# Optimization experiments

Hardware: AMD Instinct MI355X
Metric: run time of the kernel (lower is better)

Reference implementation:

```python
import jax, jax.numpy as jnp
import numpy as np

K = 20  # number of nearest neighbors (includes self, distance 0, as in torch topk(largest=False))


def edge_feature(x, k):
    """x: (B, C, N) -> edge features (B, N, k, 2C) = concat[central, neighbor - central]."""
    sq = jnp.sum(x * x, axis=1)                       # (B, N)
    inner = jnp.einsum('bcn,bcm->bnm', x, x)          # (B, N, N)
    d = sq[:, :, None] + sq[:, None, :] - 2.0 * inner # squared pairwise distance
    _, idx = jax.lax.top_k(-d, k)                     # (B, N, k) nearest indices (incl. self)
    xT = jnp.transpose(x, (0, 2, 1))                  # (B, N, C)
    # nb[b,n,j,c] = xT[b, idx[b,n,j], c]
    nb = jnp.take_along_axis(xT[:, :, None, :], idx[:, :, :, None], axis=1)  # (B, N, k, C)
    central = jnp.broadcast_to(xT[:, :, None, :], nb.shape)
    return jnp.concatenate([central, nb - central], axis=-1)  # (B, N, k, 2C)


def setup_inputs() -> dict:
    key = jax.random.key(0)
    ks = jax.random.split(key, 13)
    B, C, N = 8, 3, 4096
    def w(k_, shape, fan_in):
        return (jax.random.normal(k_, shape, dtype=jnp.float32) / np.sqrt(fan_in)).astype(jnp.float32)
    inp = {
        'x':  jax.random.normal(ks[0], (B, C, N), dtype=jnp.float32),
        # local 1x1 conv2d weights (out_ch, in_ch)
        'W1': w(ks[1], (64, 6), 6),        'b1': jnp.zeros((64,), jnp.float32),
        'W2': w(ks[2], (128, 64), 64),     'b2': jnp.zeros((128,), jnp.float32),
        # inter 1x1 conv1d
        'W3': w(ks[3], (1024, 128), 128),  'b3': jnp.zeros((1024,), jnp.float32),
        # global FC
        'W4': w(ks[4], (512, 1024), 1024), 'b4': jnp.zeros((512,), jnp.float32),
        'W5': w(ks[5], (256, 512), 512),   'b5': jnp.zeros((256,), jnp.float32),
        # final linear (torch inits this to zeros -> identity output; use small random for a
        # non-trivial correctness baseline, same math path)
        'W6': 0.01 * w(ks[6], (9, 256), 256), 'b6': jnp.zeros((9,), jnp.float32),
    }
    return inp


def reference(x, W1, b1, W2, b2, W3, b3, W4, b4, W5, b5, W6, b6):
    e = edge_feature(x, K)                                     # (B, N, k, 6)
    h = jax.nn.relu(jnp.einsum('bnkc,oc->bnko', e, W1) + b1)   # (B, N, k, 64)
    h = jax.nn.relu(jnp.einsum('bnkc,oc->bnko', h, W2) + b2)   # (B, N, k, 128)
    h = jnp.max(h, axis=2)                                     # max over k -> (B, N, 128)
    h = jax.nn.relu(jnp.einsum('bnc,oc->bno', h, W3) + b3)     # (B, N, 1024)
    g = jnp.max(h, axis=1)                                     # max over points -> (B, 1024)
    g = jax.nn.relu(g @ W4.T + b4)                             # (B, 512)
    g = jax.nn.relu(g @ W5.T + b5)                             # (B, 256)
    t = g @ W6.T + b6                                          # (B, 9)
    Bsz = x.shape[0]
    out_ch, in_ch = 3, 3
    t = t.reshape(Bsz, out_ch, in_ch) + jnp.eye(out_ch, in_ch, dtype=t.dtype)
    return t
```

## Files before the change

### kernel.cpp

```cpp
#include <hip/hip_runtime.h>
#include <hip/hip_bf16.h>
#include <cstdint>

#define B_SZ 8
#define NPTS 4096
#define KNN  20
#define NTOT (B_SZ * NPTS)
#define PPB  8

typedef unsigned int uint;
typedef unsigned short ushort;
using short8 = __attribute__((ext_vector_type(8))) short;
using f32x4  = __attribute__((ext_vector_type(4))) float;

__device__ __forceinline__ ushort f2bf(float f) {
  uint u = __float_as_uint(f);
  u += 0x7fff + ((u >> 16) & 1);
  return (ushort)(u >> 16);
}
__device__ __forceinline__ float bf2f(ushort h) {
  return __uint_as_float(((uint)h) << 16);
}

__global__ __launch_bounds__(256) void prep_kernel(const float* __restrict__ x,
                                                   const float* __restrict__ W1,
                                                   const float* __restrict__ W3,
                                                   const float* __restrict__ W2,
                                                   ushort* __restrict__ u,
                                                   ushort* __restrict__ W3b,
                                                   ushort* __restrict__ W2b) {
  int blk = blockIdx.x;
  if (blk < 1024) {
    int t = blk * 256 + threadIdx.x;
    int p = t >> 3, c0 = (t & 7) * 8;
    int b = p >> 12, n = p & (NPTS - 1);
    const float* xb = x + (size_t)b * 3 * NPTS;
    float x0 = xb[n], x1 = xb[NPTS + n], x2 = xb[2 * NPTS + n];
    uint pk[4];
    #pragma unroll
    for (int j = 0; j < 8; ++j) {
      const float* w = W1 + (c0 + j) * 6;
      float v = w[3] * x0 + w[4] * x1 + w[5] * x2;
      ushort h = f2bf(v);
      if (j & 1) pk[j >> 1] |= ((uint)h << 16); else pk[j >> 1] = h;
    }
    uint4 q; q.x = pk[0]; q.y = pk[1]; q.z = pk[2]; q.w = pk[3];
    *reinterpret_cast<uint4*>(u + (size_t)p * 64 + c0) = q;
  } else if (blk < 1088) {
    int t = (blk - 1024) * 256 + threadIdx.x;
    const float4* src = reinterpret_cast<const float4*>(W3 + t * 8);
    float4 f0 = src[0], f1 = src[1];
    uint4 pk;
    pk.x = (uint)f2bf(f0.x) | ((uint)f2bf(f0.y) << 16);
    pk.y = (uint)f2bf(f0.z) | ((uint)f2bf(f0.w) << 16);
    pk.z = (uint)f2bf(f1.x) | ((uint)f2bf(f1.y) << 16);
    pk.w = (uint)f2bf(f1.z) | ((uint)f2bf(f1.w) << 16);
    *reinterpret_cast<uint4*>(W3b + t * 8) = pk;
  } else {
    int t = (blk - 1088) * 256 + threadIdx.x;
    const float4* src = reinterpret_cast<const float4*>(W2 + t * 8);
    float4 f0 = src[0], f1 = src[1];
    uint4 pk;
    pk.x = (uint)f2bf(f0.x) | ((uint)f2bf(f0.y) << 16);
    pk.y = (uint)f2bf(f0.z) | ((uint)f2bf(f0.w) << 16);
    pk.z = (uint)f2bf(f1.x) | ((uint)f2bf(f1.y) << 16);
    pk.w = (uint)f2bf(f1.z) | ((uint)f2bf(f1.w) << 16);
    *reinterpret_cast<uint4*>(W2b + t * 8) = pk;
  }
}

__device__ __forceinline__ void sortf64(float& v, int lane) {
  #pragma unroll
  for (int k = 2; k <= 64; k <<= 1) {
    #pragma unroll
    for (int j = k >> 1; j > 0; j >>= 1) {
      float o = __shfl_xor(v, j, 64);
      bool keepmin = (((lane & k) == 0) == ((lane & j) == 0));
      bool lt = v < o;
      v = (keepmin == lt) ? v : o;
    }
  }
}

__device__ __forceinline__ void sortu64(unsigned long long& v, int lane) {
  #pragma unroll
  for (int k = 2; k <= 64; k <<= 1) {
    #pragma unroll
    for (int j = k >> 1; j > 0; j >>= 1) {
      unsigned long long o = __shfl_xor(v, j, 64);
      bool keepmin = (((lane & k) == 0) == ((lane & j) == 0));
      bool lt = v < o;
      v = (keepmin == lt) ? v : o;
    }
  }
}

__global__ __launch_bounds__(256, 4) void knn_kernel(const float* __restrict__ x,
                                                     int* __restrict__ idx_out) {
  __shared__ int surv[4][256];
  __shared__ int cnt[4];
  const unsigned long long INFK = ~0ull;
  int w = threadIdx.x >> 6, lane = threadIdx.x & 63;
  int row = blockIdx.x * 4 + w;
  int b = row >> 12, n = row & (NPTS - 1);
  const float* xb = x + (size_t)b * 3 * NPTS;
  float qx = xb[n], qy = xb[NPTS + n], qz = xb[2 * NPTS + n];
  if (lane == 0) cnt[w] = 0;

  const float4* X0 = reinterpret_cast<const float4*>(xb);
  const float4* X1 = reinterpret_cast<const float4*>(xb + NPTS);
  const float4* X2 = reinterpret_cast<const float4*>(xb + 2 * NPTS);

  uint kreg[32];
  float bm = 3.0e38f;
  #pragma unroll
  for (int i = 0; i < 16; ++i) {
    int v4 = i * 64 + lane;
    float4 a0 = X0[v4], a1 = X1[v4], a2 = X2[v4];
    float dx, dy, dz, d0, d1, d2, d3;
    dx = a0.x - qx; dy = a1.x - qy; dz = a2.x - qz; d0 = dx*dx + dy*dy + dz*dz;
    dx = a0.y - qx; dy = a1.y - qy; dz = a2.y - qz; d1 = dx*dx + dy*dy + dz*dz;
    dx = a0.z - qx; dy = a1.z - qy; dz = a2.z - qz; d2 = dx*dx + dy*dy + dz*dz;
    dx = a0.w - qx; dy = a1.w - qy; dz = a2.w - qz; d3 = dx*dx + dy*dy + dz*dz;
    bm = fminf(bm, fminf(fminf(d0, d1), fminf(d2, d3)));
    kreg[2*i]   = (__float_as_uint(d0) >> 16) | (__float_as_uint(d1) & 0xFFFF0000u);
    kreg[2*i+1] = (__float_as_uint(d2) >> 16) | (__float_as_uint(d3) & 0xFFFF0000u);
  }

  sortf64(bm, lane);
  float T = __shfl(bm, 19, 64);
  uint T16 = __float_as_uint(T) >> 16;

  asm volatile("s_waitcnt lgkmcnt(0)" ::: "memory");
  #pragma unroll
  for (int i = 0; i < 16; ++i) {
    uint ka = kreg[2*i], kb = kreg[2*i+1];
    int m0 = (i * 64 + lane) * 4;
    if ((ka & 0xffffu) <= T16) { int s = atomicAdd(&cnt[w], 1); if (s < 256) surv[w][s] = m0; }
    if ((ka >> 16)     <= T16) { int s = atomicAdd(&cnt[w], 1); if (s < 256) surv[w][s] = m0 + 1; }
    if ((kb & 0xffffu) <= T16) { int s = atomicAdd(&cnt[w], 1); if (s < 256) surv[w][s] = m0 + 2; }
    if ((kb >> 16)     <= T16) { int s = atomicAdd(&cnt[w], 1); if (s < 256) surv[w][s] = m0 + 3; }
  }
  asm volatile("s_waitcnt lgkmcnt(0)" ::: "memory");
  int M = cnt[w];

  if (M <= 256) {
    unsigned long long run = INFK;
    int nch = (M + 63) >> 6;
    for (int c = 0; c < nch; ++c) {
      int s = c * 64 + lane;
      unsigned long long v = INFK;
      if (s < M) {
        int m = surv[w][s];
        float dx = xb[m] - qx, dy = xb[NPTS + m] - qy, dz = xb[2 * NPTS + m] - qz;
        float d = dx * dx + dy * dy + dz * dz;
        v = ((unsigned long long)__float_as_uint(d) << 32) | (unsigned)m;
      }
      sortu64(v, lane);
      if (c == 0) {
        run = v;
      } else {
        unsigned long long b19 = __shfl(v, (19 - lane) & 63, 64);
        unsigned long long cand = run < b19 ? run : b19;
        run = (lane < KNN) ? cand : INFK;
        sortu64(run, lane);
      }
    }
    if (lane < KNN) idx_out[(size_t)row * KNN + lane] = (int)(run & 0xFFFFFFFFull);
  } else {
    unsigned long long prev = 0ull;
    for (int r = 0; r < KNN; ++r) {
      unsigned long long best = INFK;
      for (int i = 0; i < 16; ++i) {
        int v4 = i * 64 + lane;
        float4 a0 = X0[v4], a1 = X1[v4], a2 = X2[v4];
        float dx, dy, dz, d[4];
        dx = a0.x - qx; dy = a1.x - qy; dz = a2.x - qz; d[0] = dx*dx + dy*dy + dz*dz;
        dx = a0.y - qx; dy = a1.y - qy; dz = a2.y - qz; d[1] = dx*dx + dy*dy + dz*dz;
        dx = a0.z - qx; dy = a1.z - qy; dz = a2.z - qz; d[2] = dx*dx + dy*dy + dz*dz;
        dx = a0.w - qx; dy = a1.w - qy; dz = a2.w - qz; d[3] = dx*dx + dy*dy + dz*dz;
        #pragma unroll
        for (int j = 0; j < 4; ++j) {
          int m = i * 256 + lane * 4 + j;
          unsigned long long key =
              ((unsigned long long)__float_as_uint(d[j]) << 32) | (unsigned)m;
          if ((r == 0 || key > prev) && key < best) best = key;
        }
      }
      #pragma unroll
      for (int off = 32; off; off >>= 1) {
        unsigned long long o = __shfl_xor(best, off, 64);
        best = o < best ? o : best;
      }
      if (lane == 0) idx_out[(size_t)row * KNN + r] = (int)(best & 0xFFFFFFFFull);
      prev = best;
    }
  }
}

__global__ __launch_bounds__(256, 4) void edge_kernel(
    const float* __restrict__ x,  const float* __restrict__ W1, const float* __restrict__ b1,
    const ushort* __restrict__ W2b, const float* __restrict__ b2,
    const ushort* __restrict__ u, const int* __restrict__ idx,
    float* __restrict__ h128) {
  __shared__ __align__(16) char h1s[PPB * 32 * 128];
  __shared__ float vs[PPB * 64];
  __shared__ int   nbs[PPB * KNN];

  int tid = threadIdx.x, w = tid >> 6, l = tid & 63;
  int p0 = blockIdx.x * PPB;
  int b = p0 >> 12;
  const float* xb = x + (size_t)b * 3 * NPTS;

  for (int t = tid; t < PPB * 64; t += 256) {
    int p = t >> 6, c = t & 63;
    int n = (p0 + p) & (NPTS - 1);
    float x0 = xb[n], x1 = xb[NPTS + n], x2 = xb[2 * NPTS + n];
    const float* wr = W1 + c * 6;
    vs[t] = (wr[0] - wr[3]) * x0 + (wr[1] - wr[4]) * x1 + (wr[2] - wr[5]) * x2 + b1[c];
  }
  if (tid < PPB * KNN) nbs[tid] = idx[(size_t)p0 * KNN + tid];

  short8 bfr[8][2];
  #pragma unroll
  for (int nt = 0; nt < 8; ++nt) {
    #pragma unroll
    for (int ks = 0; ks < 2; ++ks) {
      bfr[nt][ks] = *(const short8*)(W2b + (nt * 16 + (l & 15)) * 64
                                         + ks * 32 + (l >> 4) * 8);
    }
  }
  __syncthreads();

  const ushort* ub = u + (((size_t)b) << 12) * 64;
  #pragma unroll
  for (int j = 0; j < 8; ++j) {
    int e_loc = j * 8 + (l >> 3);
    int p_loc = (w << 1) + (e_loc >> 5);
    int e_in = e_loc & 31;
    int e_src = (e_in < KNN) ? e_in : e_in - KNN;
    int nb = nbs[p_loc * KNN + e_src];
    int c0 = (l & 7) * 8;
    uint4 uv = *(const uint4*)(ub + (((size_t)nb) << 6) + c0);
    const float* vp = vs + p_loc * 64 + c0;
    float4 v0 = *(const float4*)vp, v1 = *(const float4*)(vp + 4);
    float h0 = fmaxf(bf2f((ushort)(uv.x & 0xffff)) + v0.x, 0.f);
    float h1 = fmaxf(bf2f((ushort)(uv.x >> 16))    + v0.y, 0.f);
    float h2 = fmaxf(bf2f((ushort)(uv.y & 0xffff)) + v0.z, 0.f);
    float h3 = fmaxf(bf2f((ushort)(uv.y >> 16))    + v0.w, 0.f);
    float h4 = fmaxf(bf2f((ushort)(uv.z & 0xffff)) + v1.x, 0.f);
    float h5 = fmaxf(bf2f((ushort)(uv.z >> 16))    + v1.y, 0.f);
    float h6 = fmaxf(bf2f((ushort)(uv.w & 0xffff)) + v1.z, 0.f);
    float h7 = fmaxf(bf2f((ushort)(uv.w >> 16))    + v1.w, 0.f);
    uint4 pk;
    pk.x = (uint)f2bf(h0) | ((uint)f2bf(h1) << 16);
    pk.y = (uint)f2bf(h2) | ((uint)f2bf(h3) << 16);
    pk.z = (uint)f2bf(h4) | ((uint)f2bf(h5) << 16);
    pk.w = (uint)f2bf(h6) | ((uint)f2bf(h7) << 16);
    int row = (w << 6) + e_loc;
    int byte = (row * 128 + c0 * 2) ^ ((row & 7) << 4);
    *(uint4*)(h1s + byte) = pk;
  }
  __syncthreads();

  float bias0 = b2[l], bias1 = b2[64 + l];

  #pragma unroll
  for (int pt = 0; pt < 2; ++pt) {
    int rbase = (w << 6) + (pt << 5);
    short8 a[2][2];
    #pragma unroll
    for (int m = 0; m < 2; ++m) {
      #pragma unroll
      for (int ks = 0; ks < 2; ++ks) {
        int row = rbase + m * 16 + (l & 15);
        int byte = (row * 128 + ks * 64 + (l >> 4) * 16) ^ ((row & 7) << 4);
        a[m][ks] = *(const short8*)(h1s + byte);
      }
    }
    float r03 = 0.f, r47 = 0.f;
    #pragma unroll
    for (int nt = 0; nt < 8; ++nt) {
      f32x4 acc0 = {0.f, 0.f, 0.f, 0.f}, acc1 = {0.f, 0.f, 0.f, 0.f};
      acc0 = __builtin_amdgcn_mfma_f32_16x16x32_bf16(a[0][0], bfr[nt][0], acc0, 0, 0, 0);
      acc0 = __builtin_amdgcn_mfma_f32_16x16x32_bf16(a[0][1], bfr[nt][1], acc0, 0, 0, 0);
      acc1 = __builtin_amdgcn_mfma_f32_16x16x32_bf16(a[1][0], bfr[nt][0], acc1, 0, 0, 0);
      acc1 = __builtin_amdgcn_mfma_f32_16x16x32_bf16(a[1][1], bfr[nt][1], acc1, 0, 0, 0);
      float m0 = fmaxf(fmaxf(fmaxf(acc0[0], acc1[0]), fmaxf(acc0[1], acc1[1])),
                       fmaxf(fmaxf(acc0[2], acc1[2]), fmaxf(acc0[3], acc1[3])));
      m0 = fmaxf(m0, __shfl_xor(m0, 16, 64));
      m0 = fmaxf(m0, __shfl_xor(m0, 32, 64));
      if ((l >> 4) == (nt & 3)) { if (nt < 4) r03 = m0; else r47 = m0; }
    }
    int pg = p0 + (w << 1) + pt;
    h128[(size_t)pg * 128 + l]      = fmaxf(r03 + bias0, 0.f);
    h128[(size_t)pg * 128 + 64 + l] = fmaxf(r47 + bias1, 0.f);
  }
}

__global__ __launch_bounds__(256, 2) void inter_kernel(
    const float* __restrict__ h128, const ushort* __restrict__ W3b,
    float* __restrict__ partial) {
  __shared__ __align__(16) char as_[32 * 256];
  int tid = threadIdx.x, w = tid >> 6, l = tid & 63;
  int chunk = blockIdx.x;
  const float* hp = h128 + (size_t)chunk * 32 * 128;

  {
    int row = tid >> 3, c0 = (tid & 7) * 16;
    const float4* src = reinterpret_cast<const float4*>(hp + row * 128 + c0);
    float4 f0 = src[0], f1 = src[1], f2 = src[2], f3 = src[3];
    uint4 p0, p1;
    p0.x = (uint)f2bf(f0.x) | ((uint)f2bf(f0.y) << 16);
    p0.y = (uint)f2bf(f0.z) | ((uint)f2bf(f0.w) << 16);
    p0.z = (uint)f2bf(f1.x) | ((uint)f2bf(f1.y) << 16);
    p0.w = (uint)f2bf(f1.z) | ((uint)f2bf(f1.w) << 16);
    p1.x = (uint)f2bf(f2.x) | ((uint)f2bf(f2.y) << 16);
    p1.y = (uint)f2bf(f2.z) | ((uint)f2bf(f2.w) << 16);
    p1.z = (uint)f2bf(f3.x) | ((uint)f2bf(f3.y) << 16);
    p1.w = (uint)f2bf(f3.z) | ((uint)f2bf(f3.w) << 16);
    int sw = (row & 7) << 4;
    *(uint4*)(as_ + ((row * 256 + c0 * 2) ^ sw))      = p0;
    *(uint4*)(as_ + ((row * 256 + c0 * 2 + 16) ^ sw)) = p1;
  }
  __syncthreads();

  short8 a[2][4];
  #pragma unroll
  for (int m = 0; m < 2; ++m) {
    #pragma unroll
    for (int ks = 0; ks < 4; ++ks) {
      int row = m * 16 + (l & 15);
      int byte = (row * 256 + ks * 64 + (l >> 4) * 16) ^ ((row & 7) << 4);
      a[m][ks] = *(const short8*)(as_ + byte);
    }
  }

  const ushort* wb = W3b + (size_t)(w * 256) * 128;
  float res[4];
  #pragma unroll
  for (int nt = 0; nt < 16; ++nt) {
    f32x4 acc0 = {0.f, 0.f, 0.f, 0.f}, acc1 = {0.f, 0.f, 0.f, 0.f};
    #pragma unroll
    for (int ks = 0; ks < 4; ++ks) {
      short8 bf = *(const short8*)(wb + (size_t)(nt * 16 + (l & 15)) * 128
                                      + ks * 32 + (l >> 4) * 8);
      acc0 = __builtin_amdgcn_mfma_f32_16x16x32_bf16(a[0][ks], bf, acc0, 0, 0, 0);
      acc1 = __builtin_amdgcn_mfma_f32_16x16x32_bf16(a[1][ks], bf, acc1, 0, 0, 0);
    }
    float m0 = fmaxf(fmaxf(fmaxf(acc0[0], acc1[0]), fmaxf(acc0[1], acc1[1])),
                     fmaxf(fmaxf(acc0[2], acc1[2]), fmaxf(acc0[3], acc1[3])));
    m0 = fmaxf(m0, __shfl_xor(m0, 16, 64));
    m0 = fmaxf(m0, __shfl_xor(m0, 32, 64));
    if ((l >> 4) == (nt & 3)) res[nt >> 2] = m0;
  }
  float* pp = partial + (size_t)chunk * 1024 + w * 256;
  #pragma unroll
  for (int g = 0; g < 4; ++g) pp[g * 64 + l] = res[g];
}

__global__ __launch_bounds__(256) void gmax_kernel(const float* __restrict__ partial,
                                                   const float* __restrict__ b3,
                                                   float* __restrict__ g) {
  int t = blockIdx.x * 256 + threadIdx.x;
  if (t >= B_SZ * 1024) return;
  int b = t >> 10, ch = t & 1023;
  const float* p = partial + (size_t)b * 128 * 1024 + ch;
  float m = -3.0e38f;
  for (int i = 0; i < 128; ++i) m = fmaxf(m, p[(size_t)i * 1024]);
  g[t] = fmaxf(m + b3[ch], 0.0f);
}

__global__ __launch_bounds__(64) void fc_kernel(const float* __restrict__ in,
                                                const float* __restrict__ W,
                                                const float* __restrict__ bias,
                                                float* __restrict__ out,
                                                int in_dim, int out_dim, int mode) {
  int blk = blockIdx.x;
  int b = blk / out_dim, o = blk % out_dim;
  int lane = threadIdx.x;
  const float* iv = in + (size_t)b * in_dim;
  const float* w  = W  + (size_t)o * in_dim;
  float s = 0.f;
  for (int c = lane; c < in_dim; c += 64) s += iv[c] * w[c];
  #pragma unroll
  for (int off = 32; off; off >>= 1) s += __shfl_down(s, off);
  if (lane == 0) {
    float r = s + bias[o];
    if (mode == 0) r = fmaxf(r, 0.0f);
    else if (o == 0 || o == 4 || o == 8) r += 1.0f;
    out[blk] = r;
  }
}

extern "C" void kernel_launch(void* const* d_in, const int* in_sizes, int n_in,
                              void* d_out, int out_size, void* d_ws, size_t ws_size,
                              hipStream_t stream) {
  const float* x  = (const float*)d_in[0];
  const float* W1 = (const float*)d_in[1];
  const float* b1 = (const float*)d_in[2];
  const float* W2 = (const float*)d_in[3];
  const float* b2 = (const float*)d_in[4];
  const float* W3 = (const float*)d_in[5];
  const float* b3 = (const float*)d_in[6];
  const float* W4 = (const float*)d_in[7];
  const float* b4 = (const float*)d_in[8];
  const float* W5 = (const float*)d_in[9];
  const float* b5 = (const float*)d_in[10];
  const float* W6 = (const float*)d_in[11];
  const float* b6 = (const float*)d_in[12];
  float* out = (float*)d_out;

  char* ws = (char*)d_ws;
  ushort* u_bf = (ushort*)(ws);
  int*   idxb  = (int*)  (ws + (8u  << 20));
  float* h128  = (float*)(ws + (11u << 20));
  ushort* W3b  = (ushort*)(ws + (27u << 20));
  ushort* W2b  = (ushort*)(ws + (27u << 20) + (256u << 10));
  float* part  = (float*)(ws);
  float* g     = (float*)(ws + (5u  << 20));
  float* g4    = (float*)(ws + (6u  << 20));
  float* g5    = (float*)(ws + (7u  << 20));

  hipLaunchKernelGGL(prep_kernel, dim3(1092), dim3(256), 0, stream,
                     x, W1, W3, W2, u_bf, W3b, W2b);
  hipLaunchKernelGGL(knn_kernel,  dim3(8192), dim3(256), 0, stream, x, idxb);
  hipLaunchKernelGGL(edge_kernel, dim3(NTOT / PPB), dim3(256), 0, stream,
                     x, W1, b1, W2b, b2, u_bf, idxb, h128);
  hipLaunchKernelGGL(inter_kernel, dim3(1024), dim3(256), 0, stream, h128, W3b, part);
  hipLaunchKernelGGL(gmax_kernel, dim3(32), dim3(256), 0, stream, part, b3, g);
  hipLaunchKernelGGL(fc_kernel, dim3(B_SZ * 512), dim3(64), 0, stream, g,  W4, b4, g4, 1024, 512, 0);
  hipLaunchKernelGGL(fc_kernel, dim3(B_SZ * 256), dim3(64), 0, stream, g4, W5, b5, g5, 512, 256, 0);
  hipLaunchKernelGGL(fc_kernel, dim3(B_SZ * 9),   dim3(64), 0, stream, g5, W6, b6, out, 256, 9, 1);
}
```

Before: 187.9 us.

## Fuse prep into knn launch and replace gmax kernel with atomicMax reduction

Folds the bf16 prep work into extra blocks of the knn kernel launch, so one launch is removed. The inter kernel now reduces its per-chunk maxima straight into a global buffer with atomicMax on order-preserving encoded floats, which removes the partial buffer and the separate gmax kernel. The bias and ReLU from gmax move into the first FC kernel, which decodes the values as it loads them. This adds a memset launch and atomic contention on 8K addresses, 128 chunks per batch.

```diff
diff --git a/kernel.cpp b/kernel.cpp
--- a/kernel.cpp
+++ b/kernel.cpp
@@ -21,52 +21,13 @@
 __device__ __forceinline__ float bf2f(ushort h) {
   return __uint_as_float(((uint)h) << 16);
 }
-
-__global__ __launch_bounds__(256) void prep_kernel(const float* __restrict__ x,
-                                                   const float* __restrict__ W1,
-                                                   const float* __restrict__ W3,
-                                                   const float* __restrict__ W2,
-                                                   ushort* __restrict__ u,
-                                                   ushort* __restrict__ W3b,
-                                                   ushort* __restrict__ W2b) {
-  int blk = blockIdx.x;
-  if (blk < 1024) {
-    int t = blk * 256 + threadIdx.x;
-    int p = t >> 3, c0 = (t & 7) * 8;
-    int b = p >> 12, n = p & (NPTS - 1);
-    const float* xb = x + (size_t)b * 3 * NPTS;
-    float x0 = xb[n], x1 = xb[NPTS + n], x2 = xb[2 * NPTS + n];
-    uint pk[4];
-    #pragma unroll
-    for (int j = 0; j < 8; ++j) {
-      const float* w = W1 + (c0 + j) * 6;
-      float v = w[3] * x0 + w[4] * x1 + w[5] * x2;
-      ushort h = f2bf(v);
-      if (j & 1) pk[j >> 1] |= ((uint)h << 16); else pk[j >> 1] = h;
-    }
-    uint4 q; q.x = pk[0]; q.y = pk[1]; q.z = pk[2]; q.w = pk[3];
-    *reinterpret_cast<uint4*>(u + (size_t)p * 64 + c0) = q;
-  } else if (blk < 1088) {
-    int t = (blk - 1024) * 256 + threadIdx.x;
-    const float4* src = reinterpret_cast<const float4*>(W3 + t * 8);
-    float4 f0 = src[0], f1 = src[1];
-    uint4 pk;
-    pk.x = (uint)f2bf(f0.x) | ((uint)f2bf(f0.y) << 16);
-    pk.y = (uint)f2bf(f0.z) | ((uint)f2bf(f0.w) << 16);
-    pk.z = (uint)f2bf(f1.x) | ((uint)f2bf(f1.y) << 16);
-    pk.w = (uint)f2bf(f1.z) | ((uint)f2bf(f1.w) << 16);
-    *reinterpret_cast<uint4*>(W3b + t * 8) = pk;
-  } else {
-    int t = (blk - 1088) * 256 + threadIdx.x;
-    const float4* src = reinterpret_cast<const float4*>(W2 + t * 8);
-    float4 f0 = src[0], f1 = src[1];
-    uint4 pk;
-    pk.x = (uint)f2bf(f0.x) | ((uint)f2bf(f0.y) << 16);
-    pk.y = (uint)f2bf(f0.z) | ((uint)f2bf(f0.w) << 16);
-    pk.z = (uint)f2bf(f1.x) | ((uint)f2bf(f1.y) << 16);
-    pk.w = (uint)f2bf(f1.z) | ((uint)f2bf(f1.w) << 16);
-    *reinterpret_cast<uint4*>(W2b + t * 8) = pk;
-  }
+__device__ __forceinline__ uint fenc(float f) {
+  uint u = __float_as_uint(f);
+  return (u & 0x80000000u) ? ~u : (u | 0x80000000u);
+}
+__device__ __forceinline__ float fdec(uint e) {
+  uint u = (e & 0x80000000u) ? (e & 0x7fffffffu) : ~e;
+  return __uint_as_float(u);
 }
 
 __device__ __forceinline__ void sortf64(float& v, int lane) {
@@ -95,10 +56,56 @@
   }
 }
 
-__global__ __launch_bounds__(256, 4) void knn_kernel(const float* __restrict__ x,
-                                                     int* __restrict__ idx_out) {
+__global__ __launch_bounds__(256, 4) void knn_prep_kernel(
+    const float* __restrict__ x,  const float* __restrict__ W1,
+    const float* __restrict__ W3, const float* __restrict__ W2,
+    ushort* __restrict__ u, ushort* __restrict__ W3b, ushort* __restrict__ W2b,
+    int* __restrict__ idx_out) {
   __shared__ int surv[4][256];
   __shared__ int cnt[4];
+
+  if (blockIdx.x >= 8192) {
+    int blk = blockIdx.x - 8192;
+    if (blk < 1024) {
+      int t = blk * 256 + threadIdx.x;
+      int p = t >> 3, c0 = (t & 7) * 8;
+      int b = p >> 12, n = p & (NPTS - 1);
+      const float* xb = x + (size_t)b * 3 * NPTS;
+      float x0 = xb[n], x1 = xb[NPTS + n], x2 = xb[2 * NPTS + n];
+      uint pk[4];
+      #pragma unroll
+      for (int j = 0; j < 8; ++j) {
+        const float* w = W1 + (c0 + j) * 6;
+        float v = w[3] * x0 + w[4] * x1 + w[5] * x2;
+        ushort h = f2bf(v);
+        if (j & 1) pk[j >> 1] |= ((uint)h << 16); else pk[j >> 1] = h;
+      }
+      uint4 q; q.x = pk[0]; q.y = pk[1]; q.z = pk[2]; q.w = pk[3];
+      *reinterpret_cast<uint4*>(u + (size_t)p * 64 + c0) = q;
+    } else if (blk < 1088) {
+      int t = (blk - 1024) * 256 + threadIdx.x;
+      const float4* src = reinterpret_cast<const float4*>(W3 + t * 8);
+      float4 f0 = src[0], f1 = src[1];
+      uint4 pk;
+      pk.x = (uint)f2bf(f0.x) | ((uint)f2bf(f0.y) << 16);
+      pk.y = (uint)f2bf(f0.z) | ((uint)f2bf(f0.w) << 16);
+      pk.z = (uint)f2bf(f1.x) | ((uint)f2bf(f1.y) << 16);
+      pk.w = (uint)f2bf(f1.z) | ((uint)f2bf(f1.w) << 16);
+      *reinterpret_cast<uint4*>(W3b + t * 8) = pk;
+    } else {
+      int t = (blk - 1088) * 256 + threadIdx.x;
+      const float4* src = reinterpret_cast<const float4*>(W2 + t * 8);
+      float4 f0 = src[0], f1 = src[1];
+      uint4 pk;
+      pk.x = (uint)f2bf(f0.x) | ((uint)f2bf(f0.y) << 16);
+      pk.y = (uint)f2bf(f0.z) | ((uint)f2bf(f0.w) << 16);
+      pk.z = (uint)f2bf(f1.x) | ((uint)f2bf(f1.y) << 16);
+      pk.w = (uint)f2bf(f1.z) | ((uint)f2bf(f1.w) << 16);
+      *reinterpret_cast<uint4*>(W2b + t * 8) = pk;
+    }
+    return;
+  }
+
   const unsigned long long INFK = ~0ull;
   int w = threadIdx.x >> 6, lane = threadIdx.x & 63;
   int row = blockIdx.x * 4 + w;
@@ -300,7 +307,7 @@
 
 __global__ __launch_bounds__(256, 2) void inter_kernel(
     const float* __restrict__ h128, const ushort* __restrict__ W3b,
-    float* __restrict__ partial) {
+    uint* __restrict__ g_enc) {
   __shared__ __align__(16) char as_[32 * 256];
   int tid = threadIdx.x, w = tid >> 6, l = tid & 63;
   int chunk = blockIdx.x;
@@ -354,24 +361,14 @@
     m0 = fmaxf(m0, __shfl_xor(m0, 32, 64));
     if ((l >> 4) == (nt & 3)) res[nt >> 2] = m0;
   }
-  float* pp = partial + (size_t)chunk * 1024 + w * 256;
-  #pragma unroll
-  for (int g = 0; g < 4; ++g) pp[g * 64 + l] = res[g];
-}
-
-__global__ __launch_bounds__(256) void gmax_kernel(const float* __restrict__ partial,
-                                                   const float* __restrict__ b3,
-                                                   float* __restrict__ g) {
-  int t = blockIdx.x * 256 + threadIdx.x;
-  if (t >= B_SZ * 1024) return;
-  int b = t >> 10, ch = t & 1023;
-  const float* p = partial + (size_t)b * 128 * 1024 + ch;
-  float m = -3.0e38f;
-  for (int i = 0; i < 128; ++i) m = fmaxf(m, p[(size_t)i * 1024]);
-  g[t] = fmaxf(m + b3[ch], 0.0f);
+  uint* ge = g_enc + (size_t)(chunk >> 7) * 1024 + w * 256;
+  #pragma unroll
+  for (int g = 0; g < 4; ++g) atomicMax(ge + g * 64 + l, fenc(res[g]));
 }
 
 __global__ __launch_bounds__(64) void fc_kernel(const float* __restrict__ in,
+                                                const uint* __restrict__ enc,
+                                                const float* __restrict__ pre_b,
                                                 const float* __restrict__ W,
                                                 const float* __restrict__ bias,
                                                 float* __restrict__ out,
@@ -379,15 +376,19 @@
   int blk = blockIdx.x;
   int b = blk / out_dim, o = blk % out_dim;
   int lane = threadIdx.x;
-  const float* iv = in + (size_t)b * in_dim;
-  const float* w  = W  + (size_t)o * in_dim;
+  const float* w = W + (size_t)o * in_dim;
   float s = 0.f;
-  for (int c = lane; c < in_dim; c += 64) s += iv[c] * w[c];
+  for (int c = lane; c < in_dim; c += 64) {
+    float v;
+    if (mode == 2) v = fmaxf(fdec(enc[(size_t)b * in_dim + c]) + pre_b[c], 0.f);
+    else           v = in[(size_t)b * in_dim + c];
+    s += v * w[c];
+  }
   #pragma unroll
   for (int off = 32; off; off >>= 1) s += __shfl_down(s, off);
   if (lane == 0) {
     float r = s + bias[o];
-    if (mode == 0) r = fmaxf(r, 0.0f);
+    if (mode != 1) r = fmaxf(r, 0.0f);
     else if (o == 0 || o == 4 || o == 8) r += 1.0f;
     out[blk] = r;
   }
@@ -417,19 +418,20 @@
   float* h128  = (float*)(ws + (11u << 20));
   ushort* W3b  = (ushort*)(ws + (27u << 20));
   ushort* W2b  = (ushort*)(ws + (27u << 20) + (256u << 10));
-  float* part  = (float*)(ws);
-  float* g     = (float*)(ws + (5u  << 20));
+  uint*  g_enc = (uint*) (ws + (5u  << 20));
   float* g4    = (float*)(ws + (6u  << 20));
   float* g5    = (float*)(ws + (7u  << 20));
 
-  hipLaunchKernelGGL(prep_kernel, dim3(1092), dim3(256), 0, stream,
-                     x, W1, W3, W2, u_bf, W3b, W2b);
-  hipLaunchKernelGGL(knn_kernel,  dim3(8192), dim3(256), 0, stream, x, idxb);
+  hipMemsetAsync(g_enc, 0, B_SZ * 1024 * sizeof(uint), stream);
+  hipLaunchKernelGGL(knn_prep_kernel, dim3(8192 + 1092), dim3(256), 0, stream,
+                     x, W1, W3, W2, u_bf, W3b, W2b, idxb);
   hipLaunchKernelGGL(edge_kernel, dim3(NTOT / PPB), dim3(256), 0, stream,
                      x, W1, b1, W2b, b2, u_bf, idxb, h128);
-  hipLaunchKernelGGL(inter_kernel, dim3(1024), dim3(256), 0, stream, h128, W3b, part);
-  hipLaunchKernelGGL(gmax_kernel, dim3(32), dim3(256), 0, stream, part, b3, g);
-  hipLaunchKernelGGL(fc_kernel, dim3(B_SZ * 512), dim3(64), 0, stream, g,  W4, b4, g4, 1024, 512, 0);
-  hipLaunchKernelGGL(fc_kernel, dim3(B_SZ * 256), dim3(64), 0, stream, g4, W5, b5, g5, 512, 256, 0);
-  hipLaunchKernelGGL(fc_kernel, dim3(B_SZ * 9),   dim3(64), 0, stream, g5, W6, b6, out, 256, 9, 1);
-}
+  hipLaunchKernelGGL(inter_kernel, dim3(1024), dim3(256), 0, stream, h128, W3b, g_enc);
+  hipLaunchKernelGGL(fc_kernel, dim3(B_SZ * 512), dim3(64), 0, stream,
+                     nullptr, g_enc, b3, W4, b4, g4, 1024, 512, 2);
+  hipLaunchKernelGGL(fc_kernel, dim3(B_SZ * 256), dim3(64), 0, stream,
+                     g4, nullptr, nullptr, W5, b5, g5, 512, 256, 0);
+  hipLaunchKernelGGL(fc_kernel, dim3(B_SZ * 9),   dim3(64), 0, stream,
+                     g5, nullptr, nullptr, W6, b6, out, 256, 9, 1);
+}
```

After: 189.7 us. No clear change (+1.0%).
